# Optimization experiments

Measured on AMD Instinct MI355X. Metric: run time of the kernel, lower is better.

## Reference

```python
import jax, jax.numpy as jnp
import numpy as np

LN_EPS = 1e-5

def setup_inputs() -> dict:
    key = jax.random.key(0)
    k1, k2, k3, k4 = jax.random.split(key, 4)
    B, N, D, E = 2, 50000, 128, 800000
    H = jax.random.normal(k1, (B, N, D), dtype=jnp.float32)
    src = jax.random.randint(k2, (E,), 0, N, dtype=jnp.int64)
    dst = jax.random.randint(k3, (E,), 0, N, dtype=jnp.int64)
    W = jax.random.normal(k4, (D, D), dtype=jnp.float32) * (1.0 / np.sqrt(D))
    gamma = jnp.ones((D,), dtype=jnp.float32)
    beta = jnp.zeros((D,), dtype=jnp.float32)
    return {"H": H, "src": src, "dst": dst, "W": W, "gamma": gamma, "beta": beta}

def reference(H, src, dst, W, gamma, beta):
    # m = Linear(H) (no bias): [B,N,D]
    m = jnp.einsum('bnd,de->bne', H, W)
    # gather messages at src, scatter-add into dst along node dim
    agg = jnp.zeros_like(m).at[:, dst, :].add(m[:, src, :])
    x = H + jax.nn.gelu(agg, approximate=False)
    # LayerNorm over last dim
    mu = jnp.mean(x, axis=-1, keepdims=True)
    var = jnp.var(x, axis=-1, keepdims=True)
    return (x - mu) * jax.lax.rsqrt(var + LN_EPS) * gamma + beta
```

## Files before the change

### kernel.cpp

```cpp
#include <hip/hip_runtime.h>
#include <math.h>

#define DIM 128
#define LN_EPS 1e-5f
#define CAP 64
#define TPW 2
#define FBLK 128
#define MAXB 16384

typedef unsigned short bf16_t;
typedef unsigned short u16;
typedef __attribute__((ext_vector_type(8))) short bf16x8;
typedef __attribute__((ext_vector_type(4))) float f32x4;
typedef __attribute__((ext_vector_type(2))) float f32x2;

__device__ __forceinline__ bf16_t f2bf(float f) {
    unsigned u = __builtin_bit_cast(unsigned, f);
    u += 0x7FFFu + ((u >> 16) & 1u);
    return (bf16_t)(u >> 16);
}
__device__ __forceinline__ float lo_bf(unsigned u) {
    return __builtin_bit_cast(float, u << 16);
}
__device__ __forceinline__ float hi_bf(unsigned u) {
    return __builtin_bit_cast(float, u & 0xFFFF0000u);
}

__global__ __launch_bounds__(256) void hist_prep_kernel(
    const int* __restrict__ dst, unsigned* __restrict__ hist,
    const float* __restrict__ W, bf16_t* __restrict__ WT,
    int bins4, int E, int EPB, int HB)
{
    __shared__ unsigned hb[MAXB];
    if ((int)blockIdx.x >= HB) {
        const int tid = (blockIdx.x - HB) * 256 + threadIdx.x;
        if (tid < (DIM * DIM / 4)) {
            const float4 w = ((const float4*)W)[tid];
            const int k  = tid >> 5;
            const int n0 = (tid & 31) * 4;
            WT[(n0 + 0) * DIM + k] = f2bf(w.x);
            WT[(n0 + 1) * DIM + k] = f2bf(w.y);
            WT[(n0 + 2) * DIM + k] = f2bf(w.z);
            WT[(n0 + 3) * DIM + k] = f2bf(w.w);
        }
        return;
    }
    const int b   = blockIdx.x;
    const int tid = threadIdx.x;
    const int e0  = b * EPB;
    const int e1  = (e0 + EPB < E) ? (e0 + EPB) : E;

    for (int bin0 = 0; bin0 < bins4; bin0 += MAXB) {
        const int nb = (bins4 - bin0 < MAXB) ? (bins4 - bin0) : MAXB;
        for (int i = tid; i < nb; i += 256) hb[i] = 0;
        __syncthreads();
        for (int e = e0 + tid; e < e1; e += 256) {
            const int d   = dst[e];
            const int bin = (d >> 2) - bin0;
            if (bin >= 0 && bin < nb)
                atomicAdd(&hb[bin], 1u << ((d & 3) * 8));
        }
        __syncthreads();
        for (int i = tid; i < nb; i += 256)
            hist[(size_t)b * bins4 + bin0 + i] = hb[i];
        __syncthreads();
    }
}

__global__ __launch_bounds__(256) void scan_kernel(
    const unsigned* __restrict__ hist, unsigned* __restrict__ offs,
    int* __restrict__ cursor, int bins4, int N)
{
    const int bin = blockIdx.x * 256 + threadIdx.x;
    if (bin >= bins4) return;
    unsigned l0 = 0, l1 = 0, l2 = 0, l3 = 0;
    for (int b = 0; b < FBLK; ++b) {
        const unsigned c = hist[(size_t)b * bins4 + bin];
        offs[(size_t)b * bins4 + bin] =
            (l0 & 0xFFu) | ((l1 & 0xFFu) << 8) |
            ((l2 & 0xFFu) << 16) | ((l3 & 0xFFu) << 24);
        l0 += c & 0xFFu;         l1 += (c >> 8) & 0xFFu;
        l2 += (c >> 16) & 0xFFu; l3 += (c >> 24) & 0xFFu;
    }
    const int n = bin * 4;
    if (n     < N) cursor[n]     = (int)l0;
    if (n + 1 < N) cursor[n + 1] = (int)l1;
    if (n + 2 < N) cursor[n + 2] = (int)l2;
    if (n + 3 < N) cursor[n + 3] = (int)l3;
}

__global__ __launch_bounds__(256, 2) void scatter_gemm_kernel(
    const float* __restrict__ Hmat, const bf16_t* __restrict__ WT,
    bf16_t* __restrict__ Mout,
    const int* __restrict__ src, const int* __restrict__ dst,
    const unsigned* __restrict__ offs, u16* __restrict__ eidx,
    int bins4, int nrows, int N, int E, int EPB)
{
    __shared__ unsigned hb[MAXB];
    if ((int)blockIdx.x < FBLK) {
        const int b   = blockIdx.x;
        const int tid = threadIdx.x;
        const int e0  = b * EPB;
        const int e1  = (e0 + EPB < E) ? (e0 + EPB) : E;

        for (int bin0 = 0; bin0 < bins4; bin0 += MAXB) {
            const int nb = (bins4 - bin0 < MAXB) ? (bins4 - bin0) : MAXB;
            for (int i = tid; i < nb; i += 256) hb[i] = 0;
            __syncthreads();
            for (int e = e0 + tid; e < e1; e += 256) {
                const int d   = dst[e];
                const int bin = (d >> 2) - bin0;
                if (bin >= 0 && bin < nb) {
                    const int sh = (d & 3) * 8;
                    const unsigned old = atomicAdd(&hb[bin], 1u << sh);
                    const int rank = (int)((old >> sh) & 0xFFu);
                    const int base =
                        (int)((offs[(size_t)b * bins4 + (d >> 2)] >> sh) & 0xFFu);
                    const int slot = base + rank;
                    if (slot < CAP) eidx[(size_t)d * CAP + slot] = (u16)src[e];
                }
            }
            __syncthreads();
        }
        return;
    }

    const int tid  = threadIdx.x;
    const int wave = tid >> 6;
    const int lane = tid & 63;
    const int quad = lane >> 4;
    const int l15  = lane & 15;

    bf16x8 wf[32];
    #pragma unroll
    for (int t = 0; t < 8; ++t)
        #pragma unroll
        for (int ks = 0; ks < 4; ++ks)
            wf[t * 4 + ks] = *(const bf16x8*)
                &WT[(size_t)(t * 16 + l15) * DIM + ks * 32 + quad * 8];

    const int gblock  = blockIdx.x - FBLK;
    const int baserow = (gblock * 4 + wave) * (TPW * 16);

    #pragma unroll
    for (int rt = 0; rt < TPW; ++rt) {
        const int arow = baserow + rt * 16 + l15;
        const float* Arow = Hmat + (size_t)((arow < nrows) ? arow : 0) * DIM;

        f32x4 acc[8];
        #pragma unroll
        for (int t = 0; t < 8; ++t) acc[t] = (f32x4){0.f, 0.f, 0.f, 0.f};

        #pragma unroll
        for (int ks = 0; ks < 4; ++ks) {
            const int k0 = ks * 32 + quad * 8;
            float4 a0 = *(const float4*)&Arow[k0];
            float4 a1 = *(const float4*)&Arow[k0 + 4];
            bf16x8 hf;
            hf[0] = (short)f2bf(a0.x); hf[1] = (short)f2bf(a0.y);
            hf[2] = (short)f2bf(a0.z); hf[3] = (short)f2bf(a0.w);
            hf[4] = (short)f2bf(a1.x); hf[5] = (short)f2bf(a1.y);
            hf[6] = (short)f2bf(a1.z); hf[7] = (short)f2bf(a1.w);

            #pragma unroll
            for (int t = 0; t < 8; ++t)
                acc[t] = __builtin_amdgcn_mfma_f32_16x16x32_bf16(
                             wf[t * 4 + ks], hf, acc[t], 0, 0, 0);
        }

        if (arow < nrows) {
            const int b = (arow >= N) ? 1 : 0;
            const int n = arow - (b ? N : 0);
            bf16_t* orow = Mout + ((size_t)n * 2 + b) * DIM;
            #pragma unroll
            for (int t = 0; t < 8; ++t) {
                ushort4 o;
                o.x = f2bf(acc[t][0]); o.y = f2bf(acc[t][1]);
                o.z = f2bf(acc[t][2]); o.w = f2bf(acc[t][3]);
                *(ushort4*)&orow[t * 16 + quad * 4] = o;
            }
        }
    }
}

__global__ __launch_bounds__(256, 3) void gather_kernel(
    const bf16_t* __restrict__ M, const float* __restrict__ Hmat,
    const int* __restrict__ cursor, const u16* __restrict__ eidx,
    const float* __restrict__ gamma, const float* __restrict__ beta,
    float* __restrict__ out, int N)
{
    const int wave = threadIdx.x >> 6;
    const int lane = threadIdx.x & 63;
    const int node = blockIdx.x * 4 + wave;
    if (node >= N) return;

    const int b  = lane >> 5;
    const int c4 = lane & 31;

    const size_t elembase = ((size_t)b * N + node) * DIM + c4 * 4;
    float4 h  = *(const float4*)&Hmat[elembase];
    float4 gm = *(const float4*)&gamma[c4 * 4];
    float4 bt = *(const float4*)&beta[c4 * 4];

    int cnt = cursor[node];
    if (cnt > CAP) cnt = CAP;

    int myidx = (lane < cnt) ? (int)eidx[(size_t)node * CAP + lane] : 0;

    const uint2* M2 = (const uint2*)M;
    f32x2 accA = {0.f, 0.f}, accB = {0.f, 0.f};

    int j = 0;
    for (; j + 16 <= cnt; j += 16) {
        uint2 v[16];
        #pragma unroll
        for (int q = 0; q < 16; ++q) {
            int s = __builtin_amdgcn_readlane(myidx, j + q);
            v[q] = (M2 + ((size_t)s << 6))[lane];
        }
        __builtin_amdgcn_sched_barrier(0);
        #pragma unroll
        for (int q = 0; q < 16; ++q) {
            accA += (f32x2){ lo_bf(v[q].x), hi_bf(v[q].x) };
            accB += (f32x2){ lo_bf(v[q].y), hi_bf(v[q].y) };
        }
    }
    if (j < cnt) {
        uint2 v[16];
        #pragma unroll
        for (int q = 0; q < 16; ++q) {
            int s = __builtin_amdgcn_readlane(myidx, (j + q) & 63);
            v[q] = (M2 + ((size_t)s << 6))[lane];
        }
        __builtin_amdgcn_sched_barrier(0);
        #pragma unroll
        for (int q = 0; q < 16; ++q) {
            unsigned vx = (j + q < cnt) ? v[q].x : 0u;
            unsigned vy = (j + q < cnt) ? v[q].y : 0u;
            accA += (f32x2){ lo_bf(vx), hi_bf(vx) };
            accB += (f32x2){ lo_bf(vy), hi_bf(vy) };
        }
    }
    float acc0 = accA.x, acc1 = accA.y, acc2 = accB.x, acc3 = accB.y;

    const float inv_sqrt2 = 0.70710678118654752f;
    float x0 = h.x + 0.5f * acc0 * (1.f + erff(acc0 * inv_sqrt2));
    float x1 = h.y + 0.5f * acc1 * (1.f + erff(acc1 * inv_sqrt2));
    float x2 = h.z + 0.5f * acc2 * (1.f + erff(acc2 * inv_sqrt2));
    float x3 = h.w + 0.5f * acc3 * (1.f + erff(acc3 * inv_sqrt2));

    float s  = x0 + x1 + x2 + x3;
    float ss = x0 * x0 + x1 * x1 + x2 * x2 + x3 * x3;
    #pragma unroll
    for (int o = 16; o > 0; o >>= 1) {
        s  += __shfl_xor(s,  o, 64);
        ss += __shfl_xor(ss, o, 64);
    }
    const float mean = s * (1.f / DIM);
    const float var  = ss * (1.f / DIM) - mean * mean;
    const float inv  = rsqrtf(var + LN_EPS);

    float4 o;
    o.x = (x0 - mean) * inv * gm.x + bt.x;
    o.y = (x1 - mean) * inv * gm.y + bt.y;
    o.z = (x2 - mean) * inv * gm.z + bt.z;
    o.w = (x3 - mean) * inv * gm.w + bt.w;
    *(float4*)&out[elembase] = o;
}

extern "C" void kernel_launch(void* const* d_in, const int* in_sizes, int n_in,
                              void* d_out, int out_size, void* d_ws, size_t ws_size,
                              hipStream_t stream)
{
    const float* H     = (const float*)d_in[0];
    const int*   src   = (const int*)  d_in[1];
    const int*   dst   = (const int*)  d_in[2];
    const float* W     = (const float*)d_in[3];
    const float* gamma = (const float*)d_in[4];
    const float* beta  = (const float*)d_in[5];
    float* out = (float*)d_out;

    const int E     = in_sizes[1];
    const int total = in_sizes[0];
    const int nrows = total / DIM;
    const int N     = nrows / 2;

    const int bins4 = (N + 3) / 4;
    const int EPB   = (E + FBLK - 1) / FBLK;

    char* ws = (char*)d_ws;
    bf16_t* Mbuf   = (bf16_t*)ws;   ws += (size_t)total * sizeof(bf16_t);
    int* cursor    = (int*)ws;      ws += (size_t)N * sizeof(int);
    u16* eidx      = (u16*)ws;      ws += (size_t)N * CAP * sizeof(u16);
    bf16_t* WT     = (bf16_t*)ws;   ws += (size_t)DIM * DIM * sizeof(bf16_t);
    unsigned* hist = (unsigned*)ws; ws += (size_t)FBLK * bins4 * sizeof(unsigned);
    unsigned* offs = (unsigned*)ws; ws += (size_t)FBLK * bins4 * sizeof(unsigned);

    const int PREPB = (DIM * DIM / 4 + 255) / 256;
    hist_prep_kernel<<<FBLK + PREPB, 256, 0, stream>>>(dst, hist, W, WT,
                                                       bins4, E, EPB, FBLK);

    scan_kernel<<<(bins4 + 255) / 256, 256, 0, stream>>>(hist, offs, cursor,
                                                         bins4, N);

    const int ROWS_PER_BLOCK = 4 * TPW * 16;
    const int GB = (nrows + ROWS_PER_BLOCK - 1) / ROWS_PER_BLOCK;
    scatter_gemm_kernel<<<FBLK + GB, 256, 0, stream>>>(H, WT, Mbuf, src, dst,
                                                       offs, eidx, bins4,
                                                       nrows, N, E, EPB);

    gather_kernel<<<(N + 3) / 4, 256, 0, stream>>>(Mbuf, H, cursor, eidx,
                                                   gamma, beta, out, N);
}
```

Measured before the change: 252.3 us.

## Replace fixed-capacity per-node edge slots with compact CSR row pointers

Replaces the padded N×64 per-node source index table with a compact CSR layout. A new single-block kernel prefix-sums the per-node in-degree counts into row pointers, the scatter phase writes sources at rowptr[d]+offset, and gather reads a contiguous slice. This shrinks the index buffer from N*64 to E entries and makes the index reads contiguous. In exchange it adds a serial single-block scan launch and an extra dependent rowptr load per node.

```diff
diff --git a/kernel.cpp b/kernel.cpp
--- a/kernel.cpp
+++ b/kernel.cpp
@@ -3,7 +3,6 @@
 
 #define DIM 128
 #define LN_EPS 1e-5f
-#define CAP 64
 #define TPW 2
 #define FBLK 128
 #define MAXB 16384
@@ -69,7 +68,7 @@
 
 __global__ __launch_bounds__(256) void scan_kernel(
     const unsigned* __restrict__ hist, unsigned* __restrict__ offs,
-    int* __restrict__ cursor, int bins4, int N)
+    int* __restrict__ cnt, int bins4, int N)
 {
     const int bin = blockIdx.x * 256 + threadIdx.x;
     if (bin >= bins4) return;
@@ -83,17 +82,42 @@
         l2 += (c >> 16) & 0xFFu; l3 += (c >> 24) & 0xFFu;
     }
     const int n = bin * 4;
-    if (n     < N) cursor[n]     = (int)l0;
-    if (n + 1 < N) cursor[n + 1] = (int)l1;
-    if (n + 2 < N) cursor[n + 2] = (int)l2;
-    if (n + 3 < N) cursor[n + 3] = (int)l3;
+    if (n     < N) cnt[n]     = (int)l0;
+    if (n + 1 < N) cnt[n + 1] = (int)l1;
+    if (n + 2 < N) cnt[n + 2] = (int)l2;
+    if (n + 3 < N) cnt[n + 3] = (int)l3;
+}
+
+__global__ __launch_bounds__(1024) void rowptr_kernel(
+    const int* __restrict__ cnt, int* __restrict__ rowptr, int N)
+{
+    __shared__ int ls[1024];
+    const int t     = threadIdx.x;
+    const int chunk = (N + 1023) / 1024;
+    const int i0    = t * chunk;
+    const int i1    = (i0 + chunk < N) ? (i0 + chunk) : N;
+
+    int sum = 0;
+    for (int i = i0; i < i1; ++i) sum += cnt[i];
+    ls[t] = sum;
+    __syncthreads();
+    for (int off = 1; off < 1024; off <<= 1) {
+        int v = (t >= off) ? ls[t - off] : 0;
+        __syncthreads();
+        ls[t] += v;
+        __syncthreads();
+    }
+    int run = ls[t] - sum;
+    for (int i = i0; i < i1; ++i) { rowptr[i] = run; run += cnt[i]; }
+    if (t == 1023) rowptr[N] = ls[1023];
 }
 
 __global__ __launch_bounds__(256, 2) void scatter_gemm_kernel(
     const float* __restrict__ Hmat, const bf16_t* __restrict__ WT,
     bf16_t* __restrict__ Mout,
     const int* __restrict__ src, const int* __restrict__ dst,
-    const unsigned* __restrict__ offs, u16* __restrict__ eidx,
+    const unsigned* __restrict__ offs, const int* __restrict__ rowptr,
+    u16* __restrict__ sorted_src,
     int bins4, int nrows, int N, int E, int EPB)
 {
     __shared__ unsigned hb[MAXB];
@@ -116,8 +140,8 @@
                     const int rank = (int)((old >> sh) & 0xFFu);
                     const int base =
                         (int)((offs[(size_t)b * bins4 + (d >> 2)] >> sh) & 0xFFu);
-                    const int slot = base + rank;
-                    if (slot < CAP) eidx[(size_t)d * CAP + slot] = (u16)src[e];
+                    const int pos = rowptr[d] + base + rank;
+                    sorted_src[pos] = (u16)src[e];
                 }
             }
             __syncthreads();
@@ -185,7 +209,7 @@
 
 __global__ __launch_bounds__(256, 3) void gather_kernel(
     const bf16_t* __restrict__ M, const float* __restrict__ Hmat,
-    const int* __restrict__ cursor, const u16* __restrict__ eidx,
+    const int* __restrict__ rowptr, const u16* __restrict__ sorted_src,
     const float* __restrict__ gamma, const float* __restrict__ beta,
     float* __restrict__ out, int N)
 {
@@ -202,10 +226,14 @@
     float4 gm = *(const float4*)&gamma[c4 * 4];
     float4 bt = *(const float4*)&beta[c4 * 4];
 
-    int cnt = cursor[node];
-    if (cnt > CAP) cnt = CAP;
-
-    int myidx = (lane < cnt) ? (int)eidx[(size_t)node * CAP + lane] : 0;
+    int rload = 0;
+    if (lane < 2) rload = rowptr[node + lane];
+    const int rp0 = __builtin_amdgcn_readlane(rload, 0);
+    const int rp1 = __builtin_amdgcn_readlane(rload, 1);
+    int cnt = rp1 - rp0;
+    if (cnt > 64) cnt = 64;
+
+    int myidx = (lane < cnt) ? (int)sorted_src[rp0 + lane] : 0;
 
     const uint2* M2 = (const uint2*)M;
     f32x2 accA = {0.f, 0.f}, accB = {0.f, 0.f};
@@ -289,26 +317,29 @@
     const int EPB   = (E + FBLK - 1) / FBLK;
 
     char* ws = (char*)d_ws;
-    bf16_t* Mbuf   = (bf16_t*)ws;   ws += (size_t)total * sizeof(bf16_t);
-    int* cursor    = (int*)ws;      ws += (size_t)N * sizeof(int);
-    u16* eidx      = (u16*)ws;      ws += (size_t)N * CAP * sizeof(u16);
-    bf16_t* WT     = (bf16_t*)ws;   ws += (size_t)DIM * DIM * sizeof(bf16_t);
-    unsigned* hist = (unsigned*)ws; ws += (size_t)FBLK * bins4 * sizeof(unsigned);
-    unsigned* offs = (unsigned*)ws; ws += (size_t)FBLK * bins4 * sizeof(unsigned);
+    bf16_t* Mbuf     = (bf16_t*)ws;   ws += (size_t)total * sizeof(bf16_t);
+    unsigned* hist   = (unsigned*)ws; ws += (size_t)FBLK * bins4 * sizeof(unsigned);
+    unsigned* offs   = (unsigned*)ws; ws += (size_t)FBLK * bins4 * sizeof(unsigned);
+    int* cntbuf      = (int*)ws;      ws += (size_t)N * sizeof(int);
+    int* rowptr      = (int*)ws;      ws += (size_t)(N + 1) * sizeof(int);
+    bf16_t* WT       = (bf16_t*)ws;   ws += (size_t)DIM * DIM * sizeof(bf16_t);
+    u16* sorted_src  = (u16*)ws;      ws += (size_t)(E + 64) * sizeof(u16);
 
     const int PREPB = (DIM * DIM / 4 + 255) / 256;
     hist_prep_kernel<<<FBLK + PREPB, 256, 0, stream>>>(dst, hist, W, WT,
                                                        bins4, E, EPB, FBLK);
 
-    scan_kernel<<<(bins4 + 255) / 256, 256, 0, stream>>>(hist, offs, cursor,
+    scan_kernel<<<(bins4 + 255) / 256, 256, 0, stream>>>(hist, offs, cntbuf,
                                                          bins4, N);
+
+    rowptr_kernel<<<1, 1024, 0, stream>>>(cntbuf, rowptr, N);
 
     const int ROWS_PER_BLOCK = 4 * TPW * 16;
     const int GB = (nrows + ROWS_PER_BLOCK - 1) / ROWS_PER_BLOCK;
     scatter_gemm_kernel<<<FBLK + GB, 256, 0, stream>>>(H, WT, Mbuf, src, dst,
-                                                       offs, eidx, bins4,
-                                                       nrows, N, E, EPB);
-
-    gather_kernel<<<(N + 3) / 4, 256, 0, stream>>>(Mbuf, H, cursor, eidx,
+                                                       offs, rowptr, sorted_src,
+                                                       bins4, nrows, N, E, EPB);
+
+    gather_kernel<<<(N + 3) / 4, 256, 0, stream>>>(Mbuf, H, rowptr, sorted_src,
                                                    gamma, beta, out, N);
 }
```

Result: slower. 319.3 us (+26.6%).

## Replace fixed-capacity per-node edge slots with compact CSR sorted source array

Applied to the files above, without the earlier changes.

Drops the padded N×64 per-node edge index table in favor of a compact CSR layout. The scan kernel now also computes global row offsets using a wave prefix scan plus an atomic counter, and stores (offset, count) pairs per node. The scatter writes source indices into a dense sorted array of length E, and the gather reads from that array. This shrinks the index footprint and improves locality. Row order becomes non-deterministic because of the atomic base, and the gather still caps each row at 64 edges.

```diff
diff --git a/kernel.cpp b/kernel.cpp
--- a/kernel.cpp
+++ b/kernel.cpp
@@ -3,7 +3,6 @@
 
 #define DIM 128
 #define LN_EPS 1e-5f
-#define CAP 64
 #define TPW 2
 #define FBLK 128
 #define MAXB 16384
@@ -29,11 +28,13 @@
 __global__ __launch_bounds__(256) void hist_prep_kernel(
     const int* __restrict__ dst, unsigned* __restrict__ hist,
     const float* __restrict__ W, bf16_t* __restrict__ WT,
+    int* __restrict__ gcount,
     int bins4, int E, int EPB, int HB)
 {
     __shared__ unsigned hb[MAXB];
     if ((int)blockIdx.x >= HB) {
         const int tid = (blockIdx.x - HB) * 256 + threadIdx.x;
+        if (tid == 0) *gcount = 0;
         if (tid < (DIM * DIM / 4)) {
             const float4 w = ((const float4*)W)[tid];
             const int k  = tid >> 5;
@@ -69,31 +70,54 @@
 
 __global__ __launch_bounds__(256) void scan_kernel(
     const unsigned* __restrict__ hist, unsigned* __restrict__ offs,
-    int* __restrict__ cursor, int bins4, int N)
-{
-    const int bin = blockIdx.x * 256 + threadIdx.x;
-    if (bin >= bins4) return;
+    int2* __restrict__ rowcnt, int* __restrict__ gcount, int bins4, int N)
+{
+    const int bin  = blockIdx.x * 256 + threadIdx.x;
+    const int lane = threadIdx.x & 63;
+    const bool act = (bin < bins4);
+
     unsigned l0 = 0, l1 = 0, l2 = 0, l3 = 0;
     for (int b = 0; b < FBLK; ++b) {
-        const unsigned c = hist[(size_t)b * bins4 + bin];
-        offs[(size_t)b * bins4 + bin] =
-            (l0 & 0xFFu) | ((l1 & 0xFFu) << 8) |
-            ((l2 & 0xFFu) << 16) | ((l3 & 0xFFu) << 24);
+        const unsigned c = act ? hist[(size_t)b * bins4 + bin] : 0u;
+        if (act)
+            offs[(size_t)b * bins4 + bin] =
+                (l0 & 0xFFu) | ((l1 & 0xFFu) << 8) |
+                ((l2 & 0xFFu) << 16) | ((l3 & 0xFFu) << 24);
         l0 += c & 0xFFu;         l1 += (c >> 8) & 0xFFu;
         l2 += (c >> 16) & 0xFFu; l3 += (c >> 24) & 0xFFu;
     }
-    const int n = bin * 4;
-    if (n     < N) cursor[n]     = (int)l0;
-    if (n + 1 < N) cursor[n + 1] = (int)l1;
-    if (n + 2 < N) cursor[n + 2] = (int)l2;
-    if (n + 3 < N) cursor[n + 3] = (int)l3;
+
+    const int q = (int)(l0 + l1 + l2 + l3);
+    int incl = q;
+    #pragma unroll
+    for (int off = 1; off < 64; off <<= 1) {
+        int v = __shfl_up(incl, off, 64);
+        if (lane >= off) incl += v;
+    }
+    const int excl = incl - q;
+    const int wtot = __shfl(incl, 63, 64);
+    int wbase = 0;
+    if (lane == 63) wbase = atomicAdd(gcount, wtot);
+    wbase = __shfl(wbase, 63, 64);
+    const int base = wbase + excl;
+
+    if (act) {
+        const int n = bin * 4;
+        const int b0 = base, b1 = b0 + (int)l0, b2 = b1 + (int)l1,
+                  b3 = b2 + (int)l2;
+        if (n     < N) rowcnt[n]     = make_int2(b0, (int)l0);
+        if (n + 1 < N) rowcnt[n + 1] = make_int2(b1, (int)l1);
+        if (n + 2 < N) rowcnt[n + 2] = make_int2(b2, (int)l2);
+        if (n + 3 < N) rowcnt[n + 3] = make_int2(b3, (int)l3);
+    }
 }
 
 __global__ __launch_bounds__(256, 2) void scatter_gemm_kernel(
     const float* __restrict__ Hmat, const bf16_t* __restrict__ WT,
     bf16_t* __restrict__ Mout,
     const int* __restrict__ src, const int* __restrict__ dst,
-    const unsigned* __restrict__ offs, u16* __restrict__ eidx,
+    const unsigned* __restrict__ offs, const int2* __restrict__ rowcnt,
+    u16* __restrict__ sorted_src,
     int bins4, int nrows, int N, int E, int EPB)
 {
     __shared__ unsigned hb[MAXB];
@@ -114,10 +138,10 @@
                     const int sh = (d & 3) * 8;
                     const unsigned old = atomicAdd(&hb[bin], 1u << sh);
                     const int rank = (int)((old >> sh) & 0xFFu);
-                    const int base =
+                    const int base8 =
                         (int)((offs[(size_t)b * bins4 + (d >> 2)] >> sh) & 0xFFu);
-                    const int slot = base + rank;
-                    if (slot < CAP) eidx[(size_t)d * CAP + slot] = (u16)src[e];
+                    const int pos = rowcnt[d].x + base8 + rank;
+                    sorted_src[pos] = (u16)src[e];
                 }
             }
             __syncthreads();
@@ -185,7 +209,7 @@
 
 __global__ __launch_bounds__(256, 3) void gather_kernel(
     const bf16_t* __restrict__ M, const float* __restrict__ Hmat,
-    const int* __restrict__ cursor, const u16* __restrict__ eidx,
+    const int2* __restrict__ rowcnt, const u16* __restrict__ sorted_src,
     const float* __restrict__ gamma, const float* __restrict__ beta,
     float* __restrict__ out, int N)
 {
@@ -202,10 +226,12 @@
     float4 gm = *(const float4*)&gamma[c4 * 4];
     float4 bt = *(const float4*)&beta[c4 * 4];
 
-    int cnt = cursor[node];
-    if (cnt > CAP) cnt = CAP;
-
-    int myidx = (lane < cnt) ? (int)eidx[(size_t)node * CAP + lane] : 0;
+    const int2 rc = rowcnt[node];
+    const int base = __builtin_amdgcn_readfirstlane(rc.x);
+    int cnt        = __builtin_amdgcn_readfirstlane(rc.y);
+    if (cnt > 64) cnt = 64;
+
+    int myidx = (lane < cnt) ? (int)sorted_src[base + lane] : 0;
 
     const uint2* M2 = (const uint2*)M;
     f32x2 accA = {0.f, 0.f}, accB = {0.f, 0.f};
@@ -289,26 +315,27 @@
     const int EPB   = (E + FBLK - 1) / FBLK;
 
     char* ws = (char*)d_ws;
-    bf16_t* Mbuf   = (bf16_t*)ws;   ws += (size_t)total * sizeof(bf16_t);
-    int* cursor    = (int*)ws;      ws += (size_t)N * sizeof(int);
-    u16* eidx      = (u16*)ws;      ws += (size_t)N * CAP * sizeof(u16);
-    bf16_t* WT     = (bf16_t*)ws;   ws += (size_t)DIM * DIM * sizeof(bf16_t);
-    unsigned* hist = (unsigned*)ws; ws += (size_t)FBLK * bins4 * sizeof(unsigned);
-    unsigned* offs = (unsigned*)ws; ws += (size_t)FBLK * bins4 * sizeof(unsigned);
+    bf16_t* Mbuf     = (bf16_t*)ws;   ws += (size_t)total * sizeof(bf16_t);
+    unsigned* hist   = (unsigned*)ws; ws += (size_t)FBLK * bins4 * sizeof(unsigned);
+    unsigned* offs   = (unsigned*)ws; ws += (size_t)FBLK * bins4 * sizeof(unsigned);
+    int2* rowcnt     = (int2*)ws;     ws += (size_t)N * sizeof(int2);
+    int* gcount      = (int*)ws;      ws += 256;
+    bf16_t* WT       = (bf16_t*)ws;   ws += (size_t)DIM * DIM * sizeof(bf16_t);
+    u16* sorted_src  = (u16*)ws;      ws += (size_t)(E + 64) * sizeof(u16);
 
     const int PREPB = (DIM * DIM / 4 + 255) / 256;
-    hist_prep_kernel<<<FBLK + PREPB, 256, 0, stream>>>(dst, hist, W, WT,
+    hist_prep_kernel<<<FBLK + PREPB, 256, 0, stream>>>(dst, hist, W, WT, gcount,
                                                        bins4, E, EPB, FBLK);
 
-    scan_kernel<<<(bins4 + 255) / 256, 256, 0, stream>>>(hist, offs, cursor,
-                                                         bins4, N);
+    scan_kernel<<<(bins4 + 255) / 256, 256, 0, stream>>>(hist, offs, rowcnt,
+                                                         gcount, bins4, N);
 
     const int ROWS_PER_BLOCK = 4 * TPW * 16;
     const int GB = (nrows + ROWS_PER_BLOCK - 1) / ROWS_PER_BLOCK;
     scatter_gemm_kernel<<<FBLK + GB, 256, 0, stream>>>(H, WT, Mbuf, src, dst,
-                                                       offs, eidx, bins4,
-                                                       nrows, N, E, EPB);
-
-    gather_kernel<<<(N + 3) / 4, 256, 0, stream>>>(Mbuf, H, cursor, eidx,
+                                                       offs, rowcnt, sorted_src,
+                                                       bins4, nrows, N, E, EPB);
+
+    gather_kernel<<<(N + 3) / 4, 256, 0, stream>>>(Mbuf, H, rowcnt, sorted_src,
                                                    gamma, beta, out, N);
 }
```

Measured after the change: 250.1 us. Within noise of the previous version (-0.9%).
